# Kernel optimization log

Hardware: AMD Instinct MI355X
Metric: run time of the kernel (lower is better)

Reference implementation:

```python
import jax, jax.numpy as jnp
import numpy as np

NUM_HEADS = 8
TOP_K = 32
LN_EPS = 1e-5
RENORM_EPS = 1e-5


def _split_heads(x):
    # [B, S, D] -> [B, H, S, d]
    B, S, D = x.shape
    return x.reshape(B, S, NUM_HEADS, D // NUM_HEADS).transpose(0, 2, 1, 3)


def setup_inputs() -> dict:
    key = jax.random.key(0)
    k1, k2, k3, k4 = jax.random.split(key, 4)
    B, S, D, H = 2, 2048, 1024, NUM_HEADS
    q = jax.random.normal(k1, (B, S, D), dtype=jnp.float32)
    k = jax.random.normal(k2, (B, S, D), dtype=jnp.float32)
    v = jax.random.normal(k3, (B, S, D), dtype=jnp.float32)
    attention_weight = jax.random.normal(k4, (B, H, S, S), dtype=jnp.float32)
    gamma = jnp.ones((D,), dtype=jnp.float32)
    beta = jnp.zeros((D,), dtype=jnp.float32)
    return {"q": q, "k": k, "v": v, "attention_weight": attention_weight,
            "gamma": gamma, "beta": beta}


def reference(q, k, v, attention_weight, gamma, beta):
    B, S, D = q.shape
    qh = _split_heads(q)  # [B,H,S,d]
    kh = _split_heads(k)
    vh = _split_heads(v)
    # Unscaled QK^T (faithful to source: no /sqrt(d))
    scores = jnp.einsum("bhqd,bhkd->bhqk", qh, kh)
    probs = jax.nn.softmax(scores, axis=-1)
    # top-k mask via double argsort: rank of each key by descending weight
    rank = jnp.argsort(jnp.argsort(-attention_weight, axis=-1), axis=-1)
    top_mask = (rank < TOP_K).astype(probs.dtype)
    probs = probs * top_mask
    probs = probs / (jnp.sum(probs, axis=-1, keepdims=True) + RENORM_EPS)
    out = jnp.einsum("bhqk,bhkd->bhqd", probs, vh)
    out = out.transpose(0, 2, 1, 3).reshape(B, S, D)
    # LayerNorm over last dim
    mu = jnp.mean(out, axis=-1, keepdims=True)
    var = jnp.var(out, axis=-1, keepdims=True)
    out = (out - mu) * jax.lax.rsqrt(var + LN_EPS) * gamma + beta
    return out
```

## Files before the change

### kernel.cpp

```cpp
#include <hip/hip_runtime.h>
#include <hip/hip_bf16.h>
#include <stdint.h>

#define BB 2
#define SS 2048
#define DD 1024
#define HH 8
#define HD 128
#define TOPK 32
#define ROWS (BB*HH*SS)

__global__ __launch_bounds__(256) void topk_kernel(const float* __restrict__ aw,
                                                   int* __restrict__ idx_out) {
    const int row = blockIdx.x;
    const float* p = aw + (size_t)row * SS;
    const int t = threadIdx.x;
    float4 v0 = *(const float4*)(p + 4 * t);
    float4 v1 = *(const float4*)(p + 1024 + 4 * t);
    float vals[8] = {v0.x, v0.y, v0.z, v0.w, v1.x, v1.y, v1.z, v1.w};
    unsigned long long key[8];
#pragma unroll
    for (int i = 0; i < 8; i++) {
        int e = (i < 4) ? (4 * t + i) : (1024 + 4 * t + (i - 4));
        unsigned u = __float_as_uint(vals[i]);
        unsigned sk = (u & 0x80000000u) ? ~u : (u | 0x80000000u);
        key[i] = ((unsigned long long)sk << 11) | (unsigned)(2047 - e);
    }
    __shared__ int s_cnt;
    __shared__ int s_red[4];
    __shared__ unsigned long long s_cand[256];

    unsigned thr0 = __float_as_uint(1.76f) | 0x80000000u;
    unsigned long long T = ((unsigned long long)thr0 << 11) | 2047ull;
    unsigned long long lo = 0, hi = ~0ull;
    const int lane = t & 63, wv = t >> 6;
    for (int it = 0; it < 64; ++it) {
        int c = 0;
#pragma unroll
        for (int i = 0; i < 8; i++) c += (key[i] > T) ? 1 : 0;
        for (int off = 32; off; off >>= 1) c += __shfl_down(c, off, 64);
        if (lane == 0) s_red[wv] = c;
        __syncthreads();
        int tot = s_red[0] + s_red[1] + s_red[2] + s_red[3];
        if (tot >= 32 && tot <= 192) break;
        if (tot > 192) lo = T; else hi = T;
        T = lo + ((hi - lo) >> 1);
        __syncthreads();
    }
    if (t == 0) s_cnt = 0;
    __syncthreads();
#pragma unroll
    for (int i = 0; i < 8; i++) {
        if (key[i] > T) {
            int pos = atomicAdd(&s_cnt, 1);
            if (pos < 256) s_cand[pos] = key[i];
        }
    }
    __syncthreads();
    const int C = s_cnt < 256 ? s_cnt : 256;
    if (t < 64) {
        unsigned long long c0 = (t < C) ? s_cand[t] : 0ull;
        unsigned long long c1 = (t + 64 < C) ? s_cand[t + 64] : 0ull;
        unsigned long long c2 = (t + 128 < C) ? s_cand[t + 128] : 0ull;
        unsigned long long best = c0 > c1 ? c0 : c1; if (c2 > best) best = c2;
        int* orow = idx_out + (size_t)row * TOPK;
        for (int itr = 0; itr < TOPK; ++itr) {
            unsigned long long m = best;
#pragma unroll
            for (int off = 32; off; off >>= 1) {
                unsigned long long o = __shfl_xor(m, off, 64);
                if (o > m) m = o;
            }
            if (best == m && m != 0ull) {
                orow[itr] = 2047 - (int)(m & 2047ull);
                if (c0 == m) c0 = 0; else if (c1 == m) c1 = 0; else c2 = 0;
                best = c0 > c1 ? c0 : c1; if (c2 > best) best = c2;
            }
        }
    }
}

typedef float f32x4 __attribute__((ext_vector_type(4)));
typedef _Float16 f16x8 __attribute__((ext_vector_type(8)));
typedef _Float16 f16x4 __attribute__((ext_vector_type(4)));

#define KPAD 136

__global__ __launch_bounds__(256) void stats_kernel(const float* __restrict__ q,
                                                    const float* __restrict__ k,
                                                    float* __restrict__ ws_m,
                                                    float* __restrict__ ws_l) {
    __shared__ __align__(16) _Float16 Qs[128 * KPAD];
    __shared__ __align__(16) _Float16 Ks[128 * KPAD];
    const int blk = blockIdx.x;
    const int bh = blk >> 4;
    const int qt = blk & 15;
    const int b = bh >> 3, h = bh & 7;
    const int t = threadIdx.x;
    const int wv = t >> 6, lane = t & 63;
    const int l16 = lane & 15, quad = lane >> 4;

    const float* qbase = q + ((size_t)(b * SS + qt * 128) * DD + h * HD);
#pragma unroll
    for (int i = 0; i < 16; ++i) {
        int fi = t + 256 * i;
        int r = fi >> 5, c4 = fi & 31;
        float4 f = *(const float4*)(qbase + (size_t)r * DD + c4 * 4);
        *(f16x4*)&Qs[r * KPAD + c4 * 4] =
            (f16x4){(_Float16)f.x, (_Float16)f.y, (_Float16)f.z, (_Float16)f.w};
    }
    float mrun[2][4], lrun[2][4];
#pragma unroll
    for (int a = 0; a < 2; a++)
#pragma unroll
        for (int r2 = 0; r2 < 4; r2++) { mrun[a][r2] = -INFINITY; lrun[a][r2] = 0.f; }

    const float* kbase = k + ((size_t)(b * SS) * DD + h * HD);
    for (int kt = 0; kt < 16; ++kt) {
        __syncthreads();
#pragma unroll
        for (int i = 0; i < 16; ++i) {
            int fi = t + 256 * i;
            int r = fi >> 5, c4 = fi & 31;
            float4 f = *(const float4*)(kbase + (size_t)(kt * 128 + r) * DD + c4 * 4);
            *(f16x4*)&Ks[r * KPAD + c4 * 4] =
                (f16x4){(_Float16)f.x, (_Float16)f.y, (_Float16)f.z, (_Float16)f.w};
        }
        __syncthreads();
        f32x4 acc[2][8];
#pragma unroll
        for (int a = 0; a < 2; a++)
#pragma unroll
            for (int n = 0; n < 8; n++) acc[a][n] = (f32x4){0.f, 0.f, 0.f, 0.f};
#pragma unroll
        for (int ks = 0; ks < 4; ++ks) {
            f16x8 af[2], bfr[8];
#pragma unroll
            for (int a = 0; a < 2; a++)
                af[a] = *(const f16x8*)&Qs[(wv * 32 + a * 16 + l16) * KPAD + ks * 32 + quad * 8];
#pragma unroll
            for (int n = 0; n < 8; n++)
                bfr[n] = *(const f16x8*)&Ks[(n * 16 + l16) * KPAD + ks * 32 + quad * 8];
#pragma unroll
            for (int a = 0; a < 2; a++)
#pragma unroll
                for (int n = 0; n < 8; n++)
                    acc[a][n] = __builtin_amdgcn_mfma_f32_16x16x32_f16(af[a], bfr[n], acc[a][n], 0, 0, 0);
        }
#pragma unroll
        for (int a = 0; a < 2; a++) {
#pragma unroll
            for (int r2 = 0; r2 < 4; r2++) {
                float tm = acc[a][0][r2];
#pragma unroll
                for (int n = 1; n < 8; n++) tm = fmaxf(tm, acc[a][n][r2]);
#pragma unroll
                for (int off = 1; off < 16; off <<= 1) tm = fmaxf(tm, __shfl_xor(tm, off, 64));
                float tl = 0.f;
#pragma unroll
                for (int n = 0; n < 8; n++) tl += __expf(acc[a][n][r2] - tm);
#pragma unroll
                for (int off = 1; off < 16; off <<= 1) tl += __shfl_xor(tl, off, 64);
                float mo = mrun[a][r2];
                float mn = fmaxf(mo, tm);
                lrun[a][r2] = lrun[a][r2] * __expf(mo - mn) + tl * __expf(tm - mn);
                mrun[a][r2] = mn;
            }
        }
    }
    if (l16 == 0) {
#pragma unroll
        for (int a = 0; a < 2; a++)
#pragma unroll
            for (int r2 = 0; r2 < 4; r2++) {
                int row = qt * 128 + wv * 32 + a * 16 + quad * 4 + r2;
                size_t g = (size_t)bh * SS + row;
                ws_m[g] = mrun[a][r2];
                ws_l[g] = lrun[a][r2];
            }
    }
}

__global__ __launch_bounds__(128) void attnout_kernel(const float* __restrict__ q,
                                                      const float* __restrict__ k,
                                                      const float* __restrict__ v,
                                                      const int* __restrict__ idx_ws,
                                                      const float* __restrict__ ws_m,
                                                      const float* __restrict__ ws_l,
                                                      float* __restrict__ out) {
    const int R = blockIdx.x;
    const int bh = R >> 11, s = R & 2047;
    const int b = bh >> 3, h = bh & 7;
    const int t = threadIdx.x;
    __shared__ float q_l[128];
    __shared__ int idx_l[32];
    __shared__ float e_l[32];
    __shared__ float w_l[32];
    const float* qrow = q + ((size_t)(b * SS + s) * DD + h * HD);
    q_l[t] = qrow[t];
    if (t < 32) idx_l[t] = idx_ws[(size_t)R * TOPK + t];
    __syncthreads();
    const float m = ws_m[R], Z = ws_l[R];
    const int l32 = t & 31, g = t >> 5;
    float4 q4 = *(const float4*)&q_l[l32 * 4];
    const float* kb = k + ((size_t)b * SS * DD + h * HD);
#pragma unroll
    for (int p = 0; p < 8; ++p) {
        int i = p * 4 + g;
        int ki = idx_l[i];
        float4 kv = *(const float4*)(kb + (size_t)ki * DD + l32 * 4);
        float d = q4.x * kv.x + q4.y * kv.y + q4.z * kv.z + q4.w * kv.w;
#pragma unroll
        for (int off = 1; off < 32; off <<= 1) d += __shfl_xor(d, off, 64);
        if (l32 == 0) e_l[i] = __expf(d - m);
    }
    __syncthreads();
    if (t < 32) {
        float e = e_l[t];
        float ssum = e;
#pragma unroll
        for (int off = 1; off < 32; off <<= 1) ssum += __shfl_xor(ssum, off, 64);
        float den = ssum + 1e-5f * Z;
        w_l[t] = e / den;
    }
    __syncthreads();
    const float* vb = v + ((size_t)b * SS * DD + h * HD);
    float accv = 0.f;
#pragma unroll 8
    for (int i = 0; i < 32; ++i) {
        accv += w_l[i] * vb[(size_t)idx_l[i] * DD + t];
    }
    out[((size_t)(b * SS + s) * DD) + h * HD + t] = accv;
}

__global__ __launch_bounds__(256) void ln_kernel(float* __restrict__ out,
                                                 const float* __restrict__ gamma,
                                                 const float* __restrict__ beta) {
    const int row = blockIdx.x;
    float* p = out + (size_t)row * DD;
    const int t = threadIdx.x;
    float x[4];
#pragma unroll
    for (int i = 0; i < 4; i++) x[i] = p[t + 256 * i];
    float sum = x[0] + x[1] + x[2] + x[3];
    __shared__ float red[4];
    const int lane = t & 63, wv = t >> 6;
    for (int off = 32; off; off >>= 1) sum += __shfl_down(sum, off, 64);
    if (lane == 0) red[wv] = sum;
    __syncthreads();
    float mean = (red[0] + red[1] + red[2] + red[3]) * (1.f / DD);
    __syncthreads();
    float vs = 0.f;
#pragma unroll
    for (int i = 0; i < 4; i++) { float d = x[i] - mean; vs += d * d; }
    for (int off = 32; off; off >>= 1) vs += __shfl_down(vs, off, 64);
    if (lane == 0) red[wv] = vs;
    __syncthreads();
    float var = (red[0] + red[1] + red[2] + red[3]) * (1.f / DD);
    float inv = rsqrtf(var + 1e-5f);
#pragma unroll
    for (int i = 0; i < 4; i++) {
        int c = t + 256 * i;
        p[c] = (x[i] - mean) * inv * gamma[c] + beta[c];
    }
}

extern "C" void kernel_launch(void* const* d_in, const int* in_sizes, int n_in,
                              void* d_out, int out_size, void* d_ws, size_t ws_size,
                              hipStream_t stream) {
    const float* q = (const float*)d_in[0];
    const float* k = (const float*)d_in[1];
    const float* v = (const float*)d_in[2];
    const float* aw = (const float*)d_in[3];
    const float* gamma = (const float*)d_in[4];
    const float* beta = (const float*)d_in[5];
    float* out = (float*)d_out;

    int* idx_ws = (int*)d_ws;
    float* ws_m = (float*)((char*)d_ws + (size_t)ROWS * TOPK * sizeof(int));
    float* ws_l = ws_m + ROWS;

    hipLaunchKernelGGL(topk_kernel, dim3(ROWS), dim3(256), 0, stream, aw, idx_ws);
    hipLaunchKernelGGL(stats_kernel, dim3(256), dim3(256), 0, stream, q, k, ws_m, ws_l);
    hipLaunchKernelGGL(attnout_kernel, dim3(ROWS), dim3(128), 0, stream, q, k, v, idx_ws, ws_m, ws_l, out);
    hipLaunchKernelGGL(ln_kernel, dim3(BB * SS), dim3(256), 0, stream, out, gamma, beta);
}
```

Before: 618.7 us.

## Speculative top-k threshold, rank-based output, split-K stats, head-interleaved attnout

```diff
diff --git a/kernel.cpp b/kernel.cpp
--- a/kernel.cpp
+++ b/kernel.cpp
@@ -29,24 +29,11 @@
     __shared__ int s_cnt;
     __shared__ int s_red[4];
     __shared__ unsigned long long s_cand[256];
+    const int lane = t & 63, wv = t >> 6;
 
     unsigned thr0 = __float_as_uint(1.76f) | 0x80000000u;
     unsigned long long T = ((unsigned long long)thr0 << 11) | 2047ull;
-    unsigned long long lo = 0, hi = ~0ull;
-    const int lane = t & 63, wv = t >> 6;
-    for (int it = 0; it < 64; ++it) {
-        int c = 0;
-#pragma unroll
-        for (int i = 0; i < 8; i++) c += (key[i] > T) ? 1 : 0;
-        for (int off = 32; off; off >>= 1) c += __shfl_down(c, off, 64);
-        if (lane == 0) s_red[wv] = c;
-        __syncthreads();
-        int tot = s_red[0] + s_red[1] + s_red[2] + s_red[3];
-        if (tot >= 32 && tot <= 192) break;
-        if (tot > 192) lo = T; else hi = T;
-        T = lo + ((hi - lo) >> 1);
-        __syncthreads();
-    }
+
     if (t == 0) s_cnt = 0;
     __syncthreads();
 #pragma unroll
@@ -57,26 +44,44 @@
         }
     }
     __syncthreads();
+
+    if (s_cnt < TOPK || s_cnt > 256) {
+        unsigned long long lo = 0, hi = ~0ull;
+        if (s_cnt > 256) lo = T; else hi = T;
+        T = lo + ((hi - lo) >> 1);
+        for (int it = 0; it < 40; ++it) {
+            int c = 0;
+#pragma unroll
+            for (int i = 0; i < 8; i++) c += (key[i] > T) ? 1 : 0;
+            for (int off = 32; off; off >>= 1) c += __shfl_down(c, off, 64);
+            if (lane == 0) s_red[wv] = c;
+            __syncthreads();
+            int tot = s_red[0] + s_red[1] + s_red[2] + s_red[3];
+            if (tot >= TOPK && tot <= 256) break;
+            if (tot > 256) lo = T; else hi = T;
+            T = lo + ((hi - lo) >> 1);
+            __syncthreads();
+        }
+        if (t == 0) s_cnt = 0;
+        __syncthreads();
+#pragma unroll
+        for (int i = 0; i < 8; i++) {
+            if (key[i] > T) {
+                int pos = atomicAdd(&s_cnt, 1);
+                if (pos < 256) s_cand[pos] = key[i];
+            }
+        }
+        __syncthreads();
+    }
+
     const int C = s_cnt < 256 ? s_cnt : 256;
-    if (t < 64) {
-        unsigned long long c0 = (t < C) ? s_cand[t] : 0ull;
-        unsigned long long c1 = (t + 64 < C) ? s_cand[t + 64] : 0ull;
-        unsigned long long c2 = (t + 128 < C) ? s_cand[t + 128] : 0ull;
-        unsigned long long best = c0 > c1 ? c0 : c1; if (c2 > best) best = c2;
-        int* orow = idx_out + (size_t)row * TOPK;
-        for (int itr = 0; itr < TOPK; ++itr) {
-            unsigned long long m = best;
-#pragma unroll
-            for (int off = 32; off; off >>= 1) {
-                unsigned long long o = __shfl_xor(m, off, 64);
-                if (o > m) m = o;
-            }
-            if (best == m && m != 0ull) {
-                orow[itr] = 2047 - (int)(m & 2047ull);
-                if (c0 == m) c0 = 0; else if (c1 == m) c1 = 0; else c2 = 0;
-                best = c0 > c1 ? c0 : c1; if (c2 > best) best = c2;
-            }
-        }
+    if (t < C) {
+        unsigned long long mk = s_cand[t];
+        int rank = 0;
+        for (int j = 0; j < C; ++j)
+            rank += (s_cand[j] > mk) ? 1 : 0;
+        if (rank < TOPK)
+            idx_out[(size_t)row * TOPK + rank] = 2047 - (int)(mk & 2047ull);
     }
 }
 
@@ -92,7 +97,8 @@
                                                     float* __restrict__ ws_l) {
     __shared__ __align__(16) _Float16 Qs[128 * KPAD];
     __shared__ __align__(16) _Float16 Ks[128 * KPAD];
-    const int blk = blockIdx.x;
+    const int blk = blockIdx.x & 255;
+    const int half = blockIdx.x >> 8;
     const int bh = blk >> 4;
     const int qt = blk & 15;
     const int b = bh >> 3, h = bh & 7;
@@ -116,7 +122,7 @@
         for (int r2 = 0; r2 < 4; r2++) { mrun[a][r2] = -INFINITY; lrun[a][r2] = 0.f; }
 
     const float* kbase = k + ((size_t)(b * SS) * DD + h * HD);
-    for (int kt = 0; kt < 16; ++kt) {
+    for (int kt = half * 8; kt < half * 8 + 8; ++kt) {
         __syncthreads();
 #pragma unroll
         for (int i = 0; i < 16; ++i) {
@@ -173,8 +179,8 @@
         for (int a = 0; a < 2; a++)
 #pragma unroll
             for (int r2 = 0; r2 < 4; r2++) {
-                int row = qt * 128 + wv * 32 + a * 16 + quad * 4 + r2;
-                size_t g = (size_t)bh * SS + row;
+                int rrow = qt * 128 + wv * 32 + a * 16 + quad * 4 + r2;
+                size_t g = (size_t)half * ROWS + (size_t)bh * SS + rrow;
                 ws_m[g] = mrun[a][r2];
                 ws_l[g] = lrun[a][r2];
             }
@@ -188,8 +194,9 @@
                                                       const float* __restrict__ ws_m,
                                                       const float* __restrict__ ws_l,
                                                       float* __restrict__ out) {
-    const int R = blockIdx.x;
-    const int bh = R >> 11, s = R & 2047;
+    const int bh = blockIdx.x & 15;
+    const int s = blockIdx.x >> 4;
+    const int R = (bh << 11) | s;
     const int b = bh >> 3, h = bh & 7;
     const int t = threadIdx.x;
     __shared__ float q_l[128];
@@ -200,7 +207,10 @@
     q_l[t] = qrow[t];
     if (t < 32) idx_l[t] = idx_ws[(size_t)R * TOPK + t];
     __syncthreads();
-    const float m = ws_m[R], Z = ws_l[R];
+    const float m0 = ws_m[R], m1 = ws_m[(size_t)ROWS + R];
+    const float l0 = ws_l[R], l1 = ws_l[(size_t)ROWS + R];
+    const float m = fmaxf(m0, m1);
+    const float Z = l0 * __expf(m0 - m) + l1 * __expf(m1 - m);
     const int l32 = t & 31, g = t >> 5;
     float4 q4 = *(const float4*)&q_l[l32 * 4];
     const float* kb = k + ((size_t)b * SS * DD + h * HD);
@@ -278,10 +288,10 @@
 
     int* idx_ws = (int*)d_ws;
     float* ws_m = (float*)((char*)d_ws + (size_t)ROWS * TOPK * sizeof(int));
-    float* ws_l = ws_m + ROWS;
+    float* ws_l = ws_m + 2 * ROWS;
 
     hipLaunchKernelGGL(topk_kernel, dim3(ROWS), dim3(256), 0, stream, aw, idx_ws);
-    hipLaunchKernelGGL(stats_kernel, dim3(256), dim3(256), 0, stream, q, k, ws_m, ws_l);
+    hipLaunchKernelGGL(stats_kernel, dim3(512), dim3(256), 0, stream, q, k, ws_m, ws_l);
     hipLaunchKernelGGL(attnout_kernel, dim3(ROWS), dim3(128), 0, stream, q, k, v, idx_ws, ws_m, ws_l, out);
     hipLaunchKernelGGL(ln_kernel, dim3(BB * SS), dim3(256), 0, stream, out, gamma, beta);
 }
```

Result: faster. 530.5 us (-14.3%).
